# Kernel optimization log

Hardware: AMD Instinct MI355X
Metric: run time of the kernel (lower is better)

## Reference

```python
import jax, jax.numpy as jnp
import numpy as np


def setup_inputs() -> dict:
    key = jax.random.key(0)
    ks = jax.random.split(key, 5)
    B, N, D = 8, 2048, 512
    return {
        "query": jax.random.normal(ks[0], (B, N, D), dtype=jnp.float32),
        "key": jax.random.normal(ks[1], (B, N, D), dtype=jnp.float32),
        "value": jax.random.normal(ks[2], (B, N, D), dtype=jnp.float32),
        "w_k": jax.random.normal(ks[3], (2 * N - 1, D), dtype=jnp.float32),
        "w_v": jax.random.normal(ks[4], (2 * N - 1, D), dtype=jnp.float32),
    }


def reference(query, key, value, w_k, w_v):
    B, N, D = query.shape
    # skew indices: idx[i, j] = (N-1) - i + j  maps (i,j) -> relative distance j-i,
    # distance 0 sits at the middle column (N-1) of the 2N-1 relative table.
    idx = (N - 1) - jnp.arange(N)[:, None] + jnp.arange(N)[None, :]  # [N, N]

    # content scores: [B, N, N]
    base_scores = jnp.einsum("bqd,bkd->bqk", query, key)
    # relative key scores: matmul against full 2N-1 table then skewed gather
    all_rel = jnp.einsum("bqd,rd->bqr", query, w_k)  # [B, N, 2N-1]
    rel_scores = jnp.take_along_axis(
        all_rel, jnp.broadcast_to(idx[None], (B, N, N)), axis=-1
    )
    p_attn = jax.nn.softmax(base_scores + rel_scores, axis=-1)  # [B, N, N]

    # value path: scatter probabilities into skewed [B, N, 2N-1] layout,
    # then one matmul against the relative value table (equivalent to
    # sum_j p[i,j] * w_v[(N-1)-i+j]).
    rows = jnp.arange(N)[:, None]  # [N, 1] broadcast against idx [N, N]
    p_skew = jnp.zeros((B, N, 2 * N - 1), dtype=p_attn.dtype)
    p_skew = p_skew.at[:, rows, idx].set(p_attn)
    rel_out = jnp.einsum("bqr,rd->bqd", p_skew, w_v)

    out = jnp.einsum("bqk,bkd->bqd", p_attn, value) + rel_out
    return out, p_attn
```

## Files before the change

### kernel.cpp

```cpp
#include <hip/hip_runtime.h>


#define SEQN 2048
#define DD   512
#define NB   8
#define WROWS 4095
#define WPAD  4096

typedef float     f32x4 __attribute__((ext_vector_type(4)));
typedef _Float16  h16x4 __attribute__((ext_vector_type(4)));
typedef _Float16  h16x8 __attribute__((ext_vector_type(8)));

__device__ __forceinline__ unsigned swzw(int row, int c4) {
  unsigned b = (unsigned)(row * 64 + c4 * 8);
  return b ^ (((unsigned)row & 6u) << 3);
}
__device__ __forceinline__ unsigned swzr(int row, int kg) {
  unsigned b = (unsigned)(row * 64 + kg * 16);
  return b ^ (((unsigned)row & 6u) << 3);
}

__global__ __launch_bounds__(256) void transpose_v_k(const float* __restrict__ v,
                                                     _Float16* __restrict__ vT) {
  __shared__ float tile[32][33];
  const int d0 = blockIdx.x * 32, j0 = blockIdx.y * 32, b = blockIdx.z;
  const int tid = threadIdx.x;
#pragma unroll
  for (int rep = 0; rep < 4; rep++) {
    int idx = rep * 256 + tid;
    int rr = idx >> 5, cc = idx & 31;
    tile[rr][cc] = v[((size_t)(b * SEQN + j0 + rr)) * DD + d0 + cc];
  }
  __syncthreads();
#pragma unroll
  for (int rep = 0; rep < 4; rep++) {
    int idx = rep * 256 + tid;
    int rr = idx >> 5, cc = idx & 31;
    vT[((size_t)(b * DD + d0 + rr)) * SEQN + j0 + cc] = (_Float16)tile[cc][rr];
  }
}

__global__ __launch_bounds__(256) void transpose_wv_k(const float* __restrict__ wv,
                                                      _Float16* __restrict__ wvT) {
  __shared__ float tile[32][33];
  const int d0 = blockIdx.x * 32, r0 = blockIdx.y * 32;
  const int tid = threadIdx.x;
#pragma unroll
  for (int rep = 0; rep < 4; rep++) {
    int idx = rep * 256 + tid;
    int rr = idx >> 5, cc = idx & 31;
    float val = 0.f;
    if (r0 + rr < WROWS) val = wv[(size_t)(r0 + rr) * DD + d0 + cc];
    tile[rr][cc] = val;
  }
  __syncthreads();
#pragma unroll
  for (int rep = 0; rep < 4; rep++) {
    int idx = rep * 256 + tid;
    int rr = idx >> 5, cc = idx & 31;
    wvT[(size_t)(d0 + rr) * WPAD + r0 + cc] = (_Float16)tile[cc][rr];
  }
}

__global__ __launch_bounds__(256) void score_base_k(const float* __restrict__ q,
                                                    const float* __restrict__ kmat,
                                                    float* __restrict__ S) {
  __shared__ __align__(16) char smem[16384];
  const int j0 = blockIdx.x * 128, i0 = blockIdx.y * 128, b = blockIdx.z;
  const int tid = threadIdx.x;
  const int lane = tid & 63, wave = tid >> 6;
  const int wm = wave >> 1, wn = wave & 1;
  const int r16 = lane & 15, kg = lane >> 4;

  f32x4 acc[4][4];
#pragma unroll
  for (int mf = 0; mf < 4; mf++)
#pragma unroll
    for (int nf = 0; nf < 4; nf++) acc[mf][nf] = (f32x4){0.f, 0.f, 0.f, 0.f};

  const float* qb = q + (size_t)(b * SEQN + i0) * DD;
  const float* kb = kmat + (size_t)(b * SEQN + j0) * DD;

  for (int ks = 0; ks < 16; ks++) {
    const int k0 = ks * 32;
#pragma unroll
    for (int rep = 0; rep < 4; rep++) {
      int f = rep * 256 + tid;
      int row = f >> 3, c4 = f & 7;
      f32x4 xa = *(const f32x4*)(qb + (size_t)row * DD + k0 + c4 * 4);
      f32x4 xb = *(const f32x4*)(kb + (size_t)row * DD + k0 + c4 * 4);
      h16x4 ha = {(_Float16)xa[0], (_Float16)xa[1], (_Float16)xa[2], (_Float16)xa[3]};
      h16x4 hb = {(_Float16)xb[0], (_Float16)xb[1], (_Float16)xb[2], (_Float16)xb[3]};
      *(h16x4*)(smem + swzw(row, c4)) = ha;
      *(h16x4*)(smem + 8192 + swzw(row, c4)) = hb;
    }
    __syncthreads();
    h16x8 af[4], bf[4];
#pragma unroll
    for (int mf = 0; mf < 4; mf++)
      af[mf] = *(const h16x8*)(smem + swzr(wm * 64 + mf * 16 + r16, kg));
#pragma unroll
    for (int nf = 0; nf < 4; nf++)
      bf[nf] = *(const h16x8*)(smem + 8192 + swzr(wn * 64 + nf * 16 + r16, kg));
#pragma unroll
    for (int mf = 0; mf < 4; mf++)
#pragma unroll
      for (int nf = 0; nf < 4; nf++)
        acc[mf][nf] = __builtin_amdgcn_mfma_f32_16x16x32_f16(af[mf], bf[nf], acc[mf][nf], 0, 0, 0);
    __syncthreads();
  }

#pragma unroll
  for (int mf = 0; mf < 4; mf++)
#pragma unroll
    for (int nf = 0; nf < 4; nf++)
#pragma unroll
      for (int r = 0; r < 4; r++) {
        int ii = wm * 64 + mf * 16 + kg * 4 + r;
        int jj = wn * 64 + nf * 16 + r16;
        S[(size_t)(b * SEQN + i0 + ii) * SEQN + j0 + jj] = acc[mf][nf][r];
      }
}

__global__ __launch_bounds__(256) void score_rel_k(const float* __restrict__ q,
                                                   const float* __restrict__ wk,
                                                   float* __restrict__ S) {
  __shared__ __align__(16) char smem[16384];
  const int z = blockIdx.x;
  const int i0 = blockIdx.y * 128, b = blockIdx.z;
  const int tid = threadIdx.x;
  const int lane = tid & 63, wave = tid >> 6;
  const int wm = wave >> 1, wn = wave & 1;
  const int r16 = lane & 15, kg = lane >> 4;
  const int tmin = SEQN - 128 - i0;

  f32x4 acc[4][4];
#pragma unroll
  for (int mf = 0; mf < 4; mf++)
#pragma unroll
    for (int nf = 0; nf < 4; nf++) acc[mf][nf] = (f32x4){0.f, 0.f, 0.f, 0.f};

  const float* qb = q + (size_t)(b * SEQN + i0) * DD;

  for (int ks = 0; ks < 16; ks++) {
    const int k0 = ks * 32;
#pragma unroll
    for (int rep = 0; rep < 4; rep++) {
      int f = rep * 256 + tid;
      int row = f >> 3, c4 = f & 7;
      f32x4 xa = *(const f32x4*)(qb + (size_t)row * DD + k0 + c4 * 4);
      int tr = tmin + z * 128 + row;
      if (tr > WROWS - 1) tr = WROWS - 1;
      f32x4 xb = *(const f32x4*)(wk + (size_t)tr * DD + k0 + c4 * 4);
      h16x4 ha = {(_Float16)xa[0], (_Float16)xa[1], (_Float16)xa[2], (_Float16)xa[3]};
      h16x4 hb = {(_Float16)xb[0], (_Float16)xb[1], (_Float16)xb[2], (_Float16)xb[3]};
      *(h16x4*)(smem + swzw(row, c4)) = ha;
      *(h16x4*)(smem + 8192 + swzw(row, c4)) = hb;
    }
    __syncthreads();
    h16x8 af[4], bf[4];
#pragma unroll
    for (int mf = 0; mf < 4; mf++)
      af[mf] = *(const h16x8*)(smem + swzr(wm * 64 + mf * 16 + r16, kg));
#pragma unroll
    for (int nf = 0; nf < 4; nf++)
      bf[nf] = *(const h16x8*)(smem + 8192 + swzr(wn * 64 + nf * 16 + r16, kg));
#pragma unroll
    for (int mf = 0; mf < 4; mf++)
#pragma unroll
      for (int nf = 0; nf < 4; nf++)
        acc[mf][nf] = __builtin_amdgcn_mfma_f32_16x16x32_f16(af[mf], bf[nf], acc[mf][nf], 0, 0, 0);
    __syncthreads();
  }

#pragma unroll
  for (int mf = 0; mf < 4; mf++)
#pragma unroll
    for (int nf = 0; nf < 4; nf++) {
      int bcg = z * 128 + wn * 64 + nf * 16 + r16;
#pragma unroll
      for (int r = 0; r < 4; r++) {
        int ii = wm * 64 + mf * 16 + kg * 4 + r;
        int j = bcg + ii - 127;
        if (bcg <= 2174 && j >= 0 && j < SEQN) {
          S[(size_t)(b * SEQN + i0 + ii) * SEQN + j] += acc[mf][nf][r];
        }
      }
    }
}

__global__ __launch_bounds__(256) void softmax_rows_k(float* __restrict__ S) {
  const int wid = threadIdx.x >> 6, lane = threadIdx.x & 63;
  const size_t row = (size_t)blockIdx.x * 4 + wid;
  float* p = S + row * SEQN;
  f32x4 x[8];
  float m = -3.4e38f;
#pragma unroll
  for (int c = 0; c < 8; c++) {
    x[c] = *(const f32x4*)(p + c * 256 + lane * 4);
    m = fmaxf(m, fmaxf(fmaxf(x[c][0], x[c][1]), fmaxf(x[c][2], x[c][3])));
  }
#pragma unroll
  for (int off = 32; off > 0; off >>= 1) m = fmaxf(m, __shfl_xor(m, off));
  float s = 0.f;
#pragma unroll
  for (int c = 0; c < 8; c++)
#pragma unroll
    for (int e = 0; e < 4; e++) {
      x[c][e] = __expf(x[c][e] - m);
      s += x[c][e];
    }
#pragma unroll
  for (int off = 32; off > 0; off >>= 1) s += __shfl_xor(s, off);
  float inv = 1.f / s;
#pragma unroll
  for (int c = 0; c < 8; c++) {
    x[c][0] *= inv; x[c][1] *= inv; x[c][2] *= inv; x[c][3] *= inv;
    *(f32x4*)(p + c * 256 + lane * 4) = x[c];
  }
}

__global__ __launch_bounds__(256) void out_gemm3_k(const float* __restrict__ S,
                                                   const _Float16* __restrict__ vT,
                                                   const _Float16* __restrict__ wvT,
                                                   float* __restrict__ outp) {
  __shared__ __align__(16) char smem[32768];
  const int bid = blockIdx.x;
  const int xcd = bid & 7, rr = bid >> 3;
  const int x = rr & 3, s8 = rr >> 2;
  const int sidx = xcd + 8 * s8;
  const int d0 = x * 128, i0 = (sidx & 15) * 128, b = sidx >> 4;
  const int tid = threadIdx.x, lane = tid & 63, wave = tid >> 6;
  const int wm = wave >> 1, wn = wave & 1, r16 = lane & 15, kg = lane >> 4;
  const int tmin = SEQN - 128 - i0;

  const float*    pb = S  + (size_t)(b * SEQN + i0) * SEQN;
  const _Float16* vb = vT + (size_t)(b * DD + d0) * SEQN;
  const _Float16* wb = wvT + (size_t)d0 * WPAD + tmin;

  f32x4 acc[4][4];
#pragma unroll
  for (int mf = 0; mf < 4; mf++)
#pragma unroll
    for (int nf = 0; nf < 4; nf++) acc[mf][nf] = (f32x4){0.f, 0.f, 0.f, 0.f};

  f32x4 ra[4];
  h16x4 rbv[4];

  auto LOADREGS = [&](int t) {
    if (t < 64) {
      const int k0 = t * 32;
#pragma unroll
      for (int rep = 0; rep < 4; rep++) {
        int f = rep * 256 + tid, row = f >> 3, c4 = f & 7;
        ra[rep]  = *(const f32x4*)(pb + (size_t)row * SEQN + k0 + c4 * 4);
        rbv[rep] = *(const h16x4*)(vb + (size_t)row * SEQN + k0 + c4 * 4);
      }
    } else {
      const int k0 = (t - 64) * 32;
#pragma unroll
      for (int rep = 0; rep < 4; rep++) {
        int f = rep * 256 + tid, row = f >> 3, c4 = f & 7;
        int jb = k0 + c4 * 4 + row - 127;
        const float* pr = pb + (size_t)row * SEQN;
        f32x4 v4;
#pragma unroll
        for (int e = 0; e < 4; e++) {
          int j = jb + e;
          v4[e] = (j >= 0 && j < SEQN) ? pr[j] : 0.f;
        }
        ra[rep]  = v4;
        rbv[rep] = *(const h16x4*)(wb + (size_t)row * WPAD + k0 + c4 * 4);
      }
    }
  };
  auto WRITE = [&](char* lb) {
#pragma unroll
    for (int rep = 0; rep < 4; rep++) {
      int f = rep * 256 + tid, row = f >> 3, c4 = f & 7;
      h16x4 ha = {(_Float16)ra[rep][0], (_Float16)ra[rep][1],
                  (_Float16)ra[rep][2], (_Float16)ra[rep][3]};
      *(h16x4*)(lb + swzw(row, c4)) = ha;
      *(h16x4*)(lb + 8192 + swzw(row, c4)) = rbv[rep];
    }
  };

  LOADREGS(0);
  WRITE(smem);
  LOADREGS(1);
  __syncthreads();

  for (int t = 0; t < 132; t++) {
    char* lb = smem + (t & 1) * 16384;
    if (t + 1 < 132) WRITE(smem + ((t + 1) & 1) * 16384);
    h16x8 af[4], bf[4];
#pragma unroll
    for (int mf = 0; mf < 4; mf++)
      af[mf] = *(const h16x8*)(lb + swzr(wm * 64 + mf * 16 + r16, kg));
#pragma unroll
    for (int nf = 0; nf < 4; nf++)
      bf[nf] = *(const h16x8*)(lb + 8192 + swzr(wn * 64 + nf * 16 + r16, kg));
    if (t + 2 < 132) LOADREGS(t + 2);
#pragma unroll
    for (int mf = 0; mf < 4; mf++)
#pragma unroll
      for (int nf = 0; nf < 4; nf++)
        acc[mf][nf] = __builtin_amdgcn_mfma_f32_16x16x32_f16(af[mf], bf[nf], acc[mf][nf], 0, 0, 0);
    __syncthreads();
  }

#pragma unroll
  for (int mf = 0; mf < 4; mf++)
#pragma unroll
    for (int nf = 0; nf < 4; nf++)
#pragma unroll
      for (int r = 0; r < 4; r++) {
        int ii = wm * 64 + mf * 16 + kg * 4 + r;
        int dd = wn * 64 + nf * 16 + r16;
        outp[(size_t)(b * SEQN + i0 + ii) * DD + d0 + dd] = acc[mf][nf][r];
      }
}

extern "C" void kernel_launch(void* const* d_in, const int* in_sizes, int n_in,
                              void* d_out, int out_size, void* d_ws, size_t ws_size,
                              hipStream_t stream) {
  const float* q  = (const float*)d_in[0];
  const float* k  = (const float*)d_in[1];
  const float* v  = (const float*)d_in[2];
  const float* wk = (const float*)d_in[3];
  const float* wv = (const float*)d_in[4];

  float* outp = (float*)d_out;
  float* S    = outp + (size_t)NB * SEQN * DD;

  _Float16* vT  = (_Float16*)d_ws;
  _Float16* wvT = vT + (size_t)NB * DD * SEQN;

  transpose_v_k <<<dim3(DD / 32, SEQN / 32, NB), 256, 0, stream>>>(v, vT);
  transpose_wv_k<<<dim3(DD / 32, 128),           256, 0, stream>>>(wv, wvT);
  score_base_k  <<<dim3(SEQN / 128, SEQN / 128, NB), 256, 0, stream>>>(q, k, S);
  score_rel_k   <<<dim3(17, SEQN / 128, NB),     256, 0, stream>>>(q, wk, S);
  softmax_rows_k<<<dim3(NB * SEQN / 4),          256, 0, stream>>>(S);
  out_gemm3_k   <<<dim3(512),                    256, 0, stream>>>(S, vT, wvT, outp);
}
```

Baseline: 466.7 us.

## Double-buffer LDS and prefetch global tiles in score GEMM kernels

Restructures the base and relative score GEMM kernels so the next K-tile's fp32 global loads go into registers two steps ahead. The fp16 LDS write for step t+1 goes into a second LDS buffer while MFMAs run on the current buffer. This is meant to hide global-load latency behind matrix math and remove one barrier stall per K-step. The cost is double the LDS per block and more registers, which may lower occupancy.

After: 471.8 us. Within noise of the previous version (+1.1%).

```diff
diff --git a/kernel.cpp b/kernel.cpp
--- a/kernel.cpp
+++ b/kernel.cpp
@@ -62,46 +62,62 @@
   }
 }
 
-__global__ __launch_bounds__(256) void score_base_k(const float* __restrict__ q,
-                                                    const float* __restrict__ kmat,
-                                                    float* __restrict__ S) {
-  __shared__ __align__(16) char smem[16384];
+__global__ __launch_bounds__(256) void score_base4_k(const float* __restrict__ q,
+                                                     const float* __restrict__ kmat,
+                                                     float* __restrict__ S) {
+  __shared__ __align__(16) char smem[32768];
   const int j0 = blockIdx.x * 128, i0 = blockIdx.y * 128, b = blockIdx.z;
-  const int tid = threadIdx.x;
-  const int lane = tid & 63, wave = tid >> 6;
-  const int wm = wave >> 1, wn = wave & 1;
-  const int r16 = lane & 15, kg = lane >> 4;
-
-  f32x4 acc[4][4];
-#pragma unroll
-  for (int mf = 0; mf < 4; mf++)
-#pragma unroll
-    for (int nf = 0; nf < 4; nf++) acc[mf][nf] = (f32x4){0.f, 0.f, 0.f, 0.f};
+  const int tid = threadIdx.x, lane = tid & 63, wave = tid >> 6;
+  const int wm = wave >> 1, wn = wave & 1, r16 = lane & 15, kg = lane >> 4;
 
   const float* qb = q + (size_t)(b * SEQN + i0) * DD;
   const float* kb = kmat + (size_t)(b * SEQN + j0) * DD;
 
-  for (int ks = 0; ks < 16; ks++) {
-    const int k0 = ks * 32;
-#pragma unroll
-    for (int rep = 0; rep < 4; rep++) {
-      int f = rep * 256 + tid;
-      int row = f >> 3, c4 = f & 7;
-      f32x4 xa = *(const f32x4*)(qb + (size_t)row * DD + k0 + c4 * 4);
-      f32x4 xb = *(const f32x4*)(kb + (size_t)row * DD + k0 + c4 * 4);
-      h16x4 ha = {(_Float16)xa[0], (_Float16)xa[1], (_Float16)xa[2], (_Float16)xa[3]};
-      h16x4 hb = {(_Float16)xb[0], (_Float16)xb[1], (_Float16)xb[2], (_Float16)xb[3]};
-      *(h16x4*)(smem + swzw(row, c4)) = ha;
-      *(h16x4*)(smem + 8192 + swzw(row, c4)) = hb;
-    }
-    __syncthreads();
+  f32x4 acc[4][4];
+#pragma unroll
+  for (int mf = 0; mf < 4; mf++)
+#pragma unroll
+    for (int nf = 0; nf < 4; nf++) acc[mf][nf] = (f32x4){0.f, 0.f, 0.f, 0.f};
+
+  f32x4 ra[4], rb[4];
+  auto LOADREGS = [&](int t) {
+    const int k0 = t * 32;
+#pragma unroll
+    for (int rep = 0; rep < 4; rep++) {
+      int f = rep * 256 + tid, row = f >> 3, c4 = f & 7;
+      ra[rep] = *(const f32x4*)(qb + (size_t)row * DD + k0 + c4 * 4);
+      rb[rep] = *(const f32x4*)(kb + (size_t)row * DD + k0 + c4 * 4);
+    }
+  };
+  auto WRITE = [&](char* lb) {
+#pragma unroll
+    for (int rep = 0; rep < 4; rep++) {
+      int f = rep * 256 + tid, row = f >> 3, c4 = f & 7;
+      h16x4 ha = {(_Float16)ra[rep][0], (_Float16)ra[rep][1],
+                  (_Float16)ra[rep][2], (_Float16)ra[rep][3]};
+      h16x4 hb = {(_Float16)rb[rep][0], (_Float16)rb[rep][1],
+                  (_Float16)rb[rep][2], (_Float16)rb[rep][3]};
+      *(h16x4*)(lb + swzw(row, c4)) = ha;
+      *(h16x4*)(lb + 8192 + swzw(row, c4)) = hb;
+    }
+  };
+
+  LOADREGS(0);
+  WRITE(smem);
+  LOADREGS(1);
+  __syncthreads();
+
+  for (int t = 0; t < 16; t++) {
+    char* lb = smem + (t & 1) * 16384;
+    if (t + 1 < 16) WRITE(smem + ((t + 1) & 1) * 16384);
     h16x8 af[4], bf[4];
 #pragma unroll
     for (int mf = 0; mf < 4; mf++)
-      af[mf] = *(const h16x8*)(smem + swzr(wm * 64 + mf * 16 + r16, kg));
-#pragma unroll
-    for (int nf = 0; nf < 4; nf++)
-      bf[nf] = *(const h16x8*)(smem + 8192 + swzr(wn * 64 + nf * 16 + r16, kg));
+      af[mf] = *(const h16x8*)(lb + swzr(wm * 64 + mf * 16 + r16, kg));
+#pragma unroll
+    for (int nf = 0; nf < 4; nf++)
+      bf[nf] = *(const h16x8*)(lb + 8192 + swzr(wn * 64 + nf * 16 + r16, kg));
+    if (t + 2 < 16) LOADREGS(t + 2);
 #pragma unroll
     for (int mf = 0; mf < 4; mf++)
 #pragma unroll
@@ -122,49 +138,66 @@
       }
 }
 
-__global__ __launch_bounds__(256) void score_rel_k(const float* __restrict__ q,
-                                                   const float* __restrict__ wk,
-                                                   float* __restrict__ S) {
-  __shared__ __align__(16) char smem[16384];
+__global__ __launch_bounds__(256) void score_rel4_k(const float* __restrict__ q,
+                                                    const float* __restrict__ wk,
+                                                    float* __restrict__ S) {
+  __shared__ __align__(16) char smem[32768];
   const int z = blockIdx.x;
   const int i0 = blockIdx.y * 128, b = blockIdx.z;
-  const int tid = threadIdx.x;
-  const int lane = tid & 63, wave = tid >> 6;
-  const int wm = wave >> 1, wn = wave & 1;
-  const int r16 = lane & 15, kg = lane >> 4;
+  const int tid = threadIdx.x, lane = tid & 63, wave = tid >> 6;
+  const int wm = wave >> 1, wn = wave & 1, r16 = lane & 15, kg = lane >> 4;
   const int tmin = SEQN - 128 - i0;
 
+  const float* qb = q + (size_t)(b * SEQN + i0) * DD;
+  const int tb = tmin + z * 128;
+
   f32x4 acc[4][4];
 #pragma unroll
   for (int mf = 0; mf < 4; mf++)
 #pragma unroll
     for (int nf = 0; nf < 4; nf++) acc[mf][nf] = (f32x4){0.f, 0.f, 0.f, 0.f};
 
-  const float* qb = q + (size_t)(b * SEQN + i0) * DD;
-
-  for (int ks = 0; ks < 16; ks++) {
-    const int k0 = ks * 32;
-#pragma unroll
-    for (int rep = 0; rep < 4; rep++) {
-      int f = rep * 256 + tid;
-      int row = f >> 3, c4 = f & 7;
-      f32x4 xa = *(const f32x4*)(qb + (size_t)row * DD + k0 + c4 * 4);
-      int tr = tmin + z * 128 + row;
+  f32x4 ra[4], rb[4];
+  auto LOADREGS = [&](int t) {
+    const int k0 = t * 32;
+#pragma unroll
+    for (int rep = 0; rep < 4; rep++) {
+      int f = rep * 256 + tid, row = f >> 3, c4 = f & 7;
+      ra[rep] = *(const f32x4*)(qb + (size_t)row * DD + k0 + c4 * 4);
+      int tr = tb + row;
       if (tr > WROWS - 1) tr = WROWS - 1;
-      f32x4 xb = *(const f32x4*)(wk + (size_t)tr * DD + k0 + c4 * 4);
-      h16x4 ha = {(_Float16)xa[0], (_Float16)xa[1], (_Float16)xa[2], (_Float16)xa[3]};
-      h16x4 hb = {(_Float16)xb[0], (_Float16)xb[1], (_Float16)xb[2], (_Float16)xb[3]};
-      *(h16x4*)(smem + swzw(row, c4)) = ha;
-      *(h16x4*)(smem + 8192 + swzw(row, c4)) = hb;
-    }
-    __syncthreads();
+      rb[rep] = *(const f32x4*)(wk + (size_t)tr * DD + k0 + c4 * 4);
+    }
+  };
+  auto WRITE = [&](char* lb) {
+#pragma unroll
+    for (int rep = 0; rep < 4; rep++) {
+      int f = rep * 256 + tid, row = f >> 3, c4 = f & 7;
+      h16x4 ha = {(_Float16)ra[rep][0], (_Float16)ra[rep][1],
+                  (_Float16)ra[rep][2], (_Float16)ra[rep][3]};
+      h16x4 hb = {(_Float16)rb[rep][0], (_Float16)rb[rep][1],
+                  (_Float16)rb[rep][2], (_Float16)rb[rep][3]};
+      *(h16x4*)(lb + swzw(row, c4)) = ha;
+      *(h16x4*)(lb + 8192 + swzw(row, c4)) = hb;
+    }
+  };
+
+  LOADREGS(0);
+  WRITE(smem);
+  LOADREGS(1);
+  __syncthreads();
+
+  for (int t = 0; t < 16; t++) {
+    char* lb = smem + (t & 1) * 16384;
+    if (t + 1 < 16) WRITE(smem + ((t + 1) & 1) * 16384);
     h16x8 af[4], bf[4];
 #pragma unroll
     for (int mf = 0; mf < 4; mf++)
-      af[mf] = *(const h16x8*)(smem + swzr(wm * 64 + mf * 16 + r16, kg));
-#pragma unroll
-    for (int nf = 0; nf < 4; nf++)
-      bf[nf] = *(const h16x8*)(smem + 8192 + swzr(wn * 64 + nf * 16 + r16, kg));
+      af[mf] = *(const h16x8*)(lb + swzr(wm * 64 + mf * 16 + r16, kg));
+#pragma unroll
+    for (int nf = 0; nf < 4; nf++)
+      bf[nf] = *(const h16x8*)(lb + 8192 + swzr(wn * 64 + nf * 16 + r16, kg));
+    if (t + 2 < 16) LOADREGS(t + 2);
 #pragma unroll
     for (int mf = 0; mf < 4; mf++)
 #pragma unroll
@@ -338,8 +371,8 @@
 
   transpose_v_k <<<dim3(DD / 32, SEQN / 32, NB), 256, 0, stream>>>(v, vT);
   transpose_wv_k<<<dim3(DD / 32, 128),           256, 0, stream>>>(wv, wvT);
-  score_base_k  <<<dim3(SEQN / 128, SEQN / 128, NB), 256, 0, stream>>>(q, k, S);
-  score_rel_k   <<<dim3(17, SEQN / 128, NB),     256, 0, stream>>>(q, wk, S);
+  score_base4_k <<<dim3(SEQN / 128, SEQN / 128, NB), 256, 0, stream>>>(q, k, S);
+  score_rel4_k  <<<dim3(17, SEQN / 128, NB),     256, 0, stream>>>(q, wk, S);
   softmax_rows_k<<<dim3(NB * SEQN / 4),          256, 0, stream>>>(S);
   out_gemm3_k   <<<dim3(512),                    256, 0, stream>>>(S, vT, wvT, outp);
 }
```

## Pre-convert Q/K/Wk to fp16 and double-buffer score GEMMs with direct-to-LDS loads

Applied to the files above, without the earlier changes.

Adds conversion kernels that write fp16 copies of query, key and w_k once, so the score GEMMs no longer convert fp32 to fp16 inside every tile load. Both score kernels now share a templated GEMM core that uses global_load_lds to copy tiles straight into a double-buffered, swizzled LDS layout, prefetching the next K tile while MFMAs run on the current one. This trades three extra launches and fp16 round-trip traffic for halved GEMM operand bandwidth, overlap of loads with compute, and doubled LDS per block, which may lower occupancy.

Measured after the change: 414.1 us. -11.3%, faster.

```diff
diff --git a/kernel.cpp b/kernel.cpp
--- a/kernel.cpp
+++ b/kernel.cpp
@@ -18,6 +18,93 @@
 __device__ __forceinline__ unsigned swzr(int row, int kg) {
   unsigned b = (unsigned)(row * 64 + kg * 16);
   return b ^ (((unsigned)row & 6u) << 3);
+}
+
+typedef const __attribute__((address_space(1))) unsigned int gu32_t;
+typedef __attribute__((address_space(3))) unsigned int lu32_t;
+__device__ __forceinline__ void gload_lds16(const void* g, void* l) {
+  __builtin_amdgcn_global_load_lds((gu32_t*)g, (lu32_t*)l, 16, 0, 0);
+}
+
+template <class P>
+__device__ __forceinline__ void stage_tile(const P& prov, char* smem, int buf,
+                                           int t, int wave, int l4, int cp) {
+  char* lb = smem + buf * 16384;
+#pragma unroll
+  for (int h = 0; h < 2; h++) {
+    int R = wave * 32 + h * 16;
+    int row = R + l4;
+    int c = cp ^ ((row >> 1) & 3);
+    gload_lds16((const char*)prov.a_src(t, row) + c * 16, lb + R * 64);
+    gload_lds16((const char*)prov.b_src(t, row) + c * 16, lb + 8192 + R * 64);
+  }
+}
+
+template <int NT, class P>
+__device__ __forceinline__ void gemm_core(const P& prov, char* smem, f32x4 (&acc)[4][4]) {
+  const int tid = threadIdx.x;
+  const int lane = tid & 63, wave = tid >> 6;
+  const int l4 = lane >> 2, cp = lane & 3;
+  const int wm = wave >> 1, wn = wave & 1;
+  const int r16 = lane & 15, kg = lane >> 4;
+
+  stage_tile(prov, smem, 0, 0, wave, l4, cp);
+  asm volatile("s_waitcnt vmcnt(0)" ::: "memory");
+  __builtin_amdgcn_s_barrier();
+  __builtin_amdgcn_sched_barrier(0);
+
+  int buf = 0;
+  for (int t = 0; t < NT; t++) {
+    if (t + 1 < NT) stage_tile(prov, smem, buf ^ 1, t + 1, wave, l4, cp);
+    char* lb = smem + buf * 16384;
+    h16x8 af[4], bf[4];
+#pragma unroll
+    for (int mf = 0; mf < 4; mf++)
+      af[mf] = *(const h16x8*)(lb + swzr(wm * 64 + mf * 16 + r16, kg));
+#pragma unroll
+    for (int nf = 0; nf < 4; nf++)
+      bf[nf] = *(const h16x8*)(lb + 8192 + swzr(wn * 64 + nf * 16 + r16, kg));
+#pragma unroll
+    for (int mf = 0; mf < 4; mf++)
+#pragma unroll
+      for (int nf = 0; nf < 4; nf++)
+        acc[mf][nf] = __builtin_amdgcn_mfma_f32_16x16x32_f16(af[mf], bf[nf], acc[mf][nf], 0, 0, 0);
+    asm volatile("s_waitcnt vmcnt(0)" ::: "memory");
+    __builtin_amdgcn_s_barrier();
+    __builtin_amdgcn_sched_barrier(0);
+    buf ^= 1;
+  }
+}
+
+struct ProvQK {
+  const char *ar, *br;
+  __device__ __forceinline__ const void* a_src(int t, int row) const {
+    return ar + (size_t)row * 1024 + (size_t)t * 64;
+  }
+  __device__ __forceinline__ const void* b_src(int t, int row) const {
+    return br + (size_t)row * 1024 + (size_t)t * 64;
+  }
+};
+struct ProvRel {
+  const char *ar, *wk; int tb;
+  __device__ __forceinline__ const void* a_src(int t, int row) const {
+    return ar + (size_t)row * 1024 + (size_t)t * 64;
+  }
+  __device__ __forceinline__ const void* b_src(int t, int row) const {
+    int tr = tb + row; if (tr > WROWS - 1) tr = WROWS - 1;
+    return wk + (size_t)tr * 1024 + (size_t)t * 64;
+  }
+};
+
+__global__ __launch_bounds__(256) void cvt_f16_k(const float* __restrict__ in,
+                                                 _Float16* __restrict__ out, long n8) {
+  for (long i = (long)blockIdx.x * 256 + threadIdx.x; i < n8; i += (long)gridDim.x * 256) {
+    f32x4 a = ((const f32x4*)in)[i * 2];
+    f32x4 b = ((const f32x4*)in)[i * 2 + 1];
+    h16x8 h = {(_Float16)a[0], (_Float16)a[1], (_Float16)a[2], (_Float16)a[3],
+               (_Float16)b[0], (_Float16)b[1], (_Float16)b[2], (_Float16)b[3]};
+    ((h16x8*)out)[i] = h;
+  }
 }
 
 __global__ __launch_bounds__(256) void transpose_v_k(const float* __restrict__ v,
@@ -62,15 +149,13 @@
   }
 }
 
-__global__ __launch_bounds__(256) void score_base_k(const float* __restrict__ q,
-                                                    const float* __restrict__ kmat,
-                                                    float* __restrict__ S) {
-  __shared__ __align__(16) char smem[16384];
+__global__ __launch_bounds__(256) void score_base2_k(const _Float16* __restrict__ qh,
+                                                     const _Float16* __restrict__ kh,
+                                                     float* __restrict__ S) {
+  __shared__ __align__(16) char smem[32768];
   const int j0 = blockIdx.x * 128, i0 = blockIdx.y * 128, b = blockIdx.z;
-  const int tid = threadIdx.x;
-  const int lane = tid & 63, wave = tid >> 6;
-  const int wm = wave >> 1, wn = wave & 1;
-  const int r16 = lane & 15, kg = lane >> 4;
+  const int tid = threadIdx.x, lane = tid & 63, wave = tid >> 6;
+  const int wm = wave >> 1, wn = wave & 1, r16 = lane & 15, kg = lane >> 4;
 
   f32x4 acc[4][4];
 #pragma unroll
@@ -78,37 +163,9 @@
 #pragma unroll
     for (int nf = 0; nf < 4; nf++) acc[mf][nf] = (f32x4){0.f, 0.f, 0.f, 0.f};
 
-  const float* qb = q + (size_t)(b * SEQN + i0) * DD;
-  const float* kb = kmat + (size_t)(b * SEQN + j0) * DD;
-
-  for (int ks = 0; ks < 16; ks++) {
-    const int k0 = ks * 32;
-#pragma unroll
-    for (int rep = 0; rep < 4; rep++) {
-      int f = rep * 256 + tid;
-      int row = f >> 3, c4 = f & 7;
-      f32x4 xa = *(const f32x4*)(qb + (size_t)row * DD + k0 + c4 * 4);
-      f32x4 xb = *(const f32x4*)(kb + (size_t)row * DD + k0 + c4 * 4);
-      h16x4 ha = {(_Float16)xa[0], (_Float16)xa[1], (_Float16)xa[2], (_Float16)xa[3]};
-      h16x4 hb = {(_Float16)xb[0], (_Float16)xb[1], (_Float16)xb[2], (_Float16)xb[3]};
-      *(h16x4*)(smem + swzw(row, c4)) = ha;
-      *(h16x4*)(smem + 8192 + swzw(row, c4)) = hb;
-    }
-    __syncthreads();
-    h16x8 af[4], bf[4];
-#pragma unroll
-    for (int mf = 0; mf < 4; mf++)
-      af[mf] = *(const h16x8*)(smem + swzr(wm * 64 + mf * 16 + r16, kg));
-#pragma unroll
-    for (int nf = 0; nf < 4; nf++)
-      bf[nf] = *(const h16x8*)(smem + 8192 + swzr(wn * 64 + nf * 16 + r16, kg));
-#pragma unroll
-    for (int mf = 0; mf < 4; mf++)
-#pragma unroll
-      for (int nf = 0; nf < 4; nf++)
-        acc[mf][nf] = __builtin_amdgcn_mfma_f32_16x16x32_f16(af[mf], bf[nf], acc[mf][nf], 0, 0, 0);
-    __syncthreads();
-  }
+  ProvQK prov{(const char*)(qh + (size_t)(b * SEQN + i0) * DD),
+              (const char*)(kh + (size_t)(b * SEQN + j0) * DD)};
+  gemm_core<16>(prov, smem, acc);
 
 #pragma unroll
   for (int mf = 0; mf < 4; mf++)
@@ -122,16 +179,13 @@
       }
 }
 
-__global__ __launch_bounds__(256) void score_rel_k(const float* __restrict__ q,
-                                                   const float* __restrict__ wk,
-                                                   float* __restrict__ S) {
-  __shared__ __align__(16) char smem[16384];
-  const int z = blockIdx.x;
-  const int i0 = blockIdx.y * 128, b = blockIdx.z;
-  const int tid = threadIdx.x;
-  const int lane = tid & 63, wave = tid >> 6;
-  const int wm = wave >> 1, wn = wave & 1;
-  const int r16 = lane & 15, kg = lane >> 4;
+__global__ __launch_bounds__(256) void score_rel2_k(const _Float16* __restrict__ qh,
+                                                    const _Float16* __restrict__ wkh,
+                                                    float* __restrict__ S) {
+  __shared__ __align__(16) char smem[32768];
+  const int z = blockIdx.x, i0 = blockIdx.y * 128, b = blockIdx.z;
+  const int tid = threadIdx.x, lane = tid & 63, wave = tid >> 6;
+  const int wm = wave >> 1, wn = wave & 1, r16 = lane & 15, kg = lane >> 4;
   const int tmin = SEQN - 128 - i0;
 
   f32x4 acc[4][4];
@@ -140,38 +194,9 @@
 #pragma unroll
     for (int nf = 0; nf < 4; nf++) acc[mf][nf] = (f32x4){0.f, 0.f, 0.f, 0.f};
 
-  const float* qb = q + (size_t)(b * SEQN + i0) * DD;
-
-  for (int ks = 0; ks < 16; ks++) {
-    const int k0 = ks * 32;
-#pragma unroll
-    for (int rep = 0; rep < 4; rep++) {
-      int f = rep * 256 + tid;
-      int row = f >> 3, c4 = f & 7;
-      f32x4 xa = *(const f32x4*)(qb + (size_t)row * DD + k0 + c4 * 4);
-      int tr = tmin + z * 128 + row;
-      if (tr > WROWS - 1) tr = WROWS - 1;
-      f32x4 xb = *(const f32x4*)(wk + (size_t)tr * DD + k0 + c4 * 4);
-      h16x4 ha = {(_Float16)xa[0], (_Float16)xa[1], (_Float16)xa[2], (_Float16)xa[3]};
-      h16x4 hb = {(_Float16)xb[0], (_Float16)xb[1], (_Float16)xb[2], (_Float16)xb[3]};
-      *(h16x4*)(smem + swzw(row, c4)) = ha;
-      *(h16x4*)(smem + 8192 + swzw(row, c4)) = hb;
-    }
-    __syncthreads();
-    h16x8 af[4], bf[4];
-#pragma unroll
-    for (int mf = 0; mf < 4; mf++)
-      af[mf] = *(const h16x8*)(smem + swzr(wm * 64 + mf * 16 + r16, kg));
-#pragma unroll
-    for (int nf = 0; nf < 4; nf++)
-      bf[nf] = *(const h16x8*)(smem + 8192 + swzr(wn * 64 + nf * 16 + r16, kg));
-#pragma unroll
-    for (int mf = 0; mf < 4; mf++)
-#pragma unroll
-      for (int nf = 0; nf < 4; nf++)
-        acc[mf][nf] = __builtin_amdgcn_mfma_f32_16x16x32_f16(af[mf], bf[nf], acc[mf][nf], 0, 0, 0);
-    __syncthreads();
-  }
+  ProvRel prov{(const char*)(qh + (size_t)(b * SEQN + i0) * DD),
+               (const char*)wkh, tmin + z * 128};
+  gemm_core<16>(prov, smem, acc);
 
 #pragma unroll
   for (int mf = 0; mf < 4; mf++)
@@ -182,9 +207,8 @@
       for (int r = 0; r < 4; r++) {
         int ii = wm * 64 + mf * 16 + kg * 4 + r;
         int j = bcg + ii - 127;
-        if (bcg <= 2174 && j >= 0 && j < SEQN) {
+        if (bcg <= 2174 && j >= 0 && j < SEQN)
           S[(size_t)(b * SEQN + i0 + ii) * SEQN + j] += acc[mf][nf][r];
-        }
       }
     }
 }
@@ -333,13 +357,23 @@
   float* outp = (float*)d_out;
   float* S    = outp + (size_t)NB * SEQN * DD;
 
+  const size_t nVT = (size_t)NB * DD * SEQN;
+  const size_t nWV = (size_t)DD * WPAD;
+  const size_t nQH = (size_t)NB * SEQN * DD;
   _Float16* vT  = (_Float16*)d_ws;
-  _Float16* wvT = vT + (size_t)NB * DD * SEQN;
-
+  _Float16* wvT = vT + nVT;
+  _Float16* qh  = wvT + nWV;
+  _Float16* kh  = qh + nQH;
+  _Float16* wkh = kh + nQH;
+
+  cvt_f16_k<<<dim3(2048), 256, 0, stream>>>(q,  qh,  (long)(nQH / 8));
+  cvt_f16_k<<<dim3(2048), 256, 0, stream>>>(k,  kh,  (long)(nQH / 8));
+  cvt_f16_k<<<dim3(1024), 256, 0, stream>>>(wk, wkh, (long)((size_t)WROWS * DD / 8));
   transpose_v_k <<<dim3(DD / 32, SEQN / 32, NB), 256, 0, stream>>>(v, vT);
   transpose_wv_k<<<dim3(DD / 32, 128),           256, 0, stream>>>(wv, wvT);
-  score_base_k  <<<dim3(SEQN / 128, SEQN / 128, NB), 256, 0, stream>>>(q, k, S);
-  score_rel_k   <<<dim3(17, SEQN / 128, NB),     256, 0, stream>>>(q, wk, S);
-  softmax_rows_k<<<dim3(NB * SEQN / 4),          256, 0, stream>>>(S);
-  out_gemm3_k   <<<dim3(512),                    256, 0, stream>>>(S, vT, wvT, outp);
-}
+
+  score_base2_k<<<dim3(SEQN / 128, SEQN / 128, NB), 256, 0, stream>>>(qh, kh, S);
+  score_rel2_k <<<dim3(17, SEQN / 128, NB),         256, 0, stream>>>(qh, wkh, S);
+  softmax_rows_k<<<dim3(NB * SEQN / 4),             256, 0, stream>>>(S);
+  out_gemm3_k   <<<dim3(512),                       256, 0, stream>>>(S, vT, wvT, outp);
+}
```
